# Optimization experiments

Measured on AMD Instinct MI355X. Metric: run time of the kernel, lower is better.

The kernel has to match this reference:

```python
import jax, jax.numpy as jnp
import numpy as np
import math

B, D_MODEL, SEQ_LEN, EMB_DIM, ORDER = 4, 1024, 4096, 5, 64


def setup_inputs() -> dict:
    key = jax.random.key(0)
    ks = jax.random.split(key, 12)
    L = SEQ_LEN
    # PositionalEmbedding: z = [t, Re(e^{-i f w}), Im(e^{-i f w})]
    t = jnp.linspace(0.0, 1.0, L)[None, :, None]                      # [1,L,1]
    bands = (EMB_DIM - 1) // 2
    t_rescaled = jnp.linspace(0.0, L - 1, L)[None, :, None]           # [1,L,1]
    w = 2 * math.pi * t_rescaled / L
    f = jnp.linspace(1e-4, bands - 1, bands)[None, None]              # [1,1,bands]
    zc = jnp.exp(-1j * f * w.astype(jnp.complex64))                   # [1,L,bands]
    z = jnp.concatenate([t, zc.real, zc.imag], axis=-1)               # [1,L,EMB_DIM]
    # ExponentialModulation deltas (fast_decay_pct=0.3, slow_decay_pct=1.5, target=0.01)
    max_decay = math.log(0.01) / 0.3
    min_decay = math.log(0.01) / 1.5
    deltas = jnp.linspace(min_decay, max_decay, D_MODEL)[None, None]  # [1,1,D]
    s = 0.1  # small init scale for MLP weights
    return {
        "x": jax.random.normal(ks[0], (B, D_MODEL, SEQ_LEN), jnp.float32),
        "L": SEQ_LEN,
        "z": z.astype(jnp.float32),
        "t": t.astype(jnp.float32),
        "deltas": deltas.astype(jnp.float32),
        "W1": jax.random.normal(ks[1], (ORDER, EMB_DIM), jnp.float32) * s,
        "b1": jax.random.normal(ks[2], (ORDER,), jnp.float32) * s,
        "freq": jnp.ones((1, ORDER), jnp.float32),  # Sin freq, w=1
        "W2": jax.random.normal(ks[3], (ORDER, ORDER), jnp.float32) * s,
        "b2": jax.random.normal(ks[4], (ORDER,), jnp.float32) * s,
        "W3": jax.random.normal(ks[5], (ORDER, ORDER), jnp.float32) * s,
        "b3": jax.random.normal(ks[6], (ORDER,), jnp.float32) * s,
        "W4": jax.random.normal(ks[7], (D_MODEL, ORDER), jnp.float32) * s,
        "bias": jax.random.normal(ks[8], (D_MODEL,), jnp.float32),
    }


def reference(x, L, z, t, deltas, W1, b1, freq, W2, b2, W3, b3, W4, bias):
    # --- implicit filter MLP: z [1,L,E] -> k [1,L,D] ---
    zL, tL = z[:, :L], t[:, :L]
    h = jnp.sin(freq * (jnp.einsum('ble,oe->blo', zL, W1) + b1))
    h = jnp.sin(freq * (jnp.einsum('blo,po->blp', h, W2) + b2))
    h = jnp.sin(freq * (jnp.einsum('blo,po->blp', h, W3) + b3))
    h = jnp.einsum('blo,do->bld', h, W4)                # [1,L,D], no bias
    # --- exponential modulation ---
    decay = jnp.exp(-tL * jnp.abs(deltas))              # [1,L,D]
    h = h * decay
    k = h[0].T                                          # [D, L] per-channel filters
    # --- FFT causal conv: irfft(rfft(u)*rfft(k)/n, norm='forward') == plain circular conv on 2L ---
    n = 2 * L
    u_f = jnp.fft.rfft(x, n=n)                          # [B,D,L+1] complex
    k_f = jnp.fft.rfft(k, n=n)                          # [D,L+1]
    y = jnp.fft.irfft(u_f * k_f, n=n)[..., :L]          # [B,D,L]
    out = y + x * bias[:, None]                         # D.unsqueeze(-1) bias term, gelu=False
    return out.astype(x.dtype)
```

## Files before the change

kernel.cpp:

```cpp
#include <hip/hip_runtime.h>
#include <math.h>


#define PAD(i) ((i) + ((i) >> 4))
#define TWO_PI 6.2831853071795864769f

typedef float2 cplx;

__device__ __forceinline__ cplx cmul(cplx a, cplx b) {
    return make_float2(a.x * b.x - a.y * b.y, a.x * b.y + a.y * b.x);
}

__device__ __forceinline__ void dft8(cplx v[8], float sgn) {
    cplx t;
    t = v[1]; v[1] = v[4]; v[4] = t;
    t = v[3]; v[3] = v[6]; v[6] = t;
#pragma unroll
    for (int i = 0; i < 8; i += 2) {
        cplx a = v[i], b = v[i + 1];
        v[i]     = make_float2(a.x + b.x, a.y + b.y);
        v[i + 1] = make_float2(a.x - b.x, a.y - b.y);
    }
#pragma unroll
    for (int i = 0; i < 8; i += 4) {
        cplx a = v[i], b = v[i + 2];
        v[i]     = make_float2(a.x + b.x, a.y + b.y);
        v[i + 2] = make_float2(a.x - b.x, a.y - b.y);
        cplx c1 = v[i + 1], d = v[i + 3];
        cplx dt = make_float2(-sgn * d.y, sgn * d.x);
        v[i + 1] = make_float2(c1.x + dt.x, c1.y + dt.y);
        v[i + 3] = make_float2(c1.x - dt.x, c1.y - dt.y);
    }
    const float C = 0.70710678118654752440f;
    cplx a, b, bt;
    a = v[0]; b = v[4];
    v[0] = make_float2(a.x + b.x, a.y + b.y);
    v[4] = make_float2(a.x - b.x, a.y - b.y);
    a = v[1]; b = v[5]; bt = cmul(b, make_float2(C, sgn * C));
    v[1] = make_float2(a.x + bt.x, a.y + bt.y);
    v[5] = make_float2(a.x - bt.x, a.y - bt.y);
    a = v[2]; b = v[6]; bt = make_float2(-sgn * b.y, sgn * b.x);
    v[2] = make_float2(a.x + bt.x, a.y + bt.y);
    v[6] = make_float2(a.x - bt.x, a.y - bt.y);
    a = v[3]; b = v[7]; bt = cmul(b, make_float2(-C, sgn * C));
    v[3] = make_float2(a.x + bt.x, a.y + bt.y);
    v[7] = make_float2(a.x - bt.x, a.y - bt.y);
}

__device__ __forceinline__ void twiddle_powers(float ang, cplx w[8]) {
    float s, c;
    __sincosf(ang, &s, &c);
    w[1] = make_float2(c, s);
    w[2] = cmul(w[1], w[1]);
    w[3] = cmul(w[2], w[1]);
    w[4] = cmul(w[2], w[2]);
    w[5] = cmul(w[4], w[1]);
    w[6] = cmul(w[3], w[3]);
    w[7] = cmul(w[4], w[3]);
}

template <int NS>
__device__ __forceinline__ void fft_pass_ip(cplx* __restrict__ buf, int j, float sgn) {
    cplx* rp = buf + (j + (j >> 4));
    cplx v[8];
#pragma unroll
    for (int r = 0; r < 8; r++) v[r] = rp[544 * r];
    if (NS > 1) {
        int jm = j & (NS - 1);
        float ang = sgn * (TWO_PI / (float)(NS * 8)) * (float)jm;
        cplx w[8];
        twiddle_powers(ang, w);
#pragma unroll
        for (int r = 1; r < 8; r++) v[r] = cmul(v[r], w[r]);
    }
    dft8(v, sgn);
    __syncthreads();
    int base = ((j & ~(NS - 1)) << 3) + (j & (NS - 1));
    cplx* wp = buf + (base + (base >> 4));
#pragma unroll
    for (int r = 0; r < 8; r++) {
        const int off = (NS == 1) ? r
                      : (NS == 8) ? (8 * r + (r >> 1))
                      : (NS == 64) ? (68 * r)
                      : (544 * r);
        wp[off] = v[r];
    }
    __syncthreads();
}

__device__ __forceinline__ void fft_pass1_fwd_regs(cplx* __restrict__ buf, int j,
                                                   const cplx xv[4]) {
    cplx v[8];
#pragma unroll
    for (int r = 0; r < 4; r++) v[r] = xv[r];
#pragma unroll
    for (int r = 4; r < 8; r++) v[r] = make_float2(0.f, 0.f);
    dft8(v, -1.0f);
    int b8 = 8 * j;
    cplx* wp = buf + (b8 + (b8 >> 4));
#pragma unroll
    for (int r = 0; r < 8; r++) wp[r] = v[r];
    __syncthreads();
}

__global__ __launch_bounds__(256) void mlp_kernel(
    const float* __restrict__ zin, const float* __restrict__ W1,
    const float* __restrict__ b1, const float* __restrict__ freq,
    const float* __restrict__ W2, const float* __restrict__ b2,
    const float* __restrict__ W3, const float* __restrict__ b3,
    float* __restrict__ h3T) {
    __shared__ float hs1[64][64];
    __shared__ float hs2[64][64];
    int tid = threadIdx.x;
    int l = tid & 63, w = tid >> 6;
    int lg = blockIdx.x * 64 + l;

    float zf[5];
#pragma unroll
    for (int e = 0; e < 5; e++) zf[e] = zin[lg * 5 + e];

#pragma unroll
    for (int i = 0; i < 16; i++) {
        int o = w * 16 + i;
        float a = b1[o];
#pragma unroll
        for (int e = 0; e < 5; e++) a += W1[o * 5 + e] * zf[e];
        hs1[o][l] = __sinf(freq[o] * a);
    }
    __syncthreads();

    float acc[16];
#pragma unroll
    for (int i = 0; i < 16; i++) acc[i] = b2[w * 16 + i];
#pragma unroll 8
    for (int o = 0; o < 64; o++) {
        float hv = hs1[o][l];
#pragma unroll
        for (int i = 0; i < 16; i++) acc[i] += W2[(w * 16 + i) * 64 + o] * hv;
    }
#pragma unroll
    for (int i = 0; i < 16; i++)
        hs2[w * 16 + i][l] = __sinf(freq[w * 16 + i] * acc[i]);
    __syncthreads();

#pragma unroll
    for (int i = 0; i < 16; i++) acc[i] = b3[w * 16 + i];
#pragma unroll 8
    for (int o = 0; o < 64; o++) {
        float hv = hs2[o][l];
#pragma unroll
        for (int i = 0; i < 16; i++) acc[i] += W3[(w * 16 + i) * 64 + o] * hv;
    }
#pragma unroll
    for (int i = 0; i < 16; i++)
        h3T[(size_t)(w * 16 + i) * 4096 + lg] = __sinf(freq[w * 16 + i] * acc[i]);
}

__global__ __launch_bounds__(256) void kgemm_kernel(
    const float* __restrict__ h3T, const float* __restrict__ W4,
    const float* __restrict__ tvec, const float* __restrict__ deltas,
    float* __restrict__ kout) {
    int lt = blockIdx.x & 3;
    int dt = blockIdx.x >> 2;
    int l0 = lt * 1024 + threadIdx.x * 4;
    float4 acc[16];
#pragma unroll
    for (int i = 0; i < 16; i++) acc[i] = make_float4(0.f, 0.f, 0.f, 0.f);
#pragma unroll 8
    for (int o = 0; o < 64; o++) {
        float4 h = *(const float4*)(h3T + (size_t)o * 4096 + l0);
#pragma unroll
        for (int i = 0; i < 16; i++) {
            float wv = W4[(size_t)(dt * 16 + i) * 64 + o];
            acc[i].x += wv * h.x; acc[i].y += wv * h.y;
            acc[i].z += wv * h.z; acc[i].w += wv * h.w;
        }
    }
    float4 tl = *(const float4*)(tvec + l0);
#pragma unroll
    for (int i = 0; i < 16; i++) {
        int d = dt * 16 + i;
        float da = fabsf(deltas[d]);
        float4 o;
        o.x = acc[i].x * __expf(-tl.x * da);
        o.y = acc[i].y * __expf(-tl.y * da);
        o.z = acc[i].z * __expf(-tl.z * da);
        o.w = acc[i].w * __expf(-tl.w * da);
        *(float4*)(kout + (size_t)d * 4096 + l0) = o;
    }
}

__global__ __launch_bounds__(512) void convf_kernel(
    const float* __restrict__ x, const float* __restrict__ kin,
    const float* __restrict__ bias, float* __restrict__ out) {
    __shared__ cplx buf[4352];
    int d = blockIdx.x;
    int t = threadIdx.x;

    float sb, cb;
    __sincosf(-TWO_PI * (float)t * (1.0f / 8192.0f), &sb, &cb);
    cplx wk[4];
    wk[0] = make_float2(cb, sb);
    wk[1] = cmul(wk[0], make_float2(0.92387953251128675613f, -0.38268343236508977173f));
    wk[2] = cmul(wk[0], make_float2(0.70710678118654752440f, -0.70710678118654752440f));
    wk[3] = cmul(wk[0], make_float2(0.38268343236508977173f, -0.92387953251128675613f));

    cplx* rb  = buf + (t + (t >> 4));
    cplx* qb2 = buf + (((4096 - t) + ((4096 - t) >> 4)) - 1632);

    {
        const cplx* k2 = (const cplx*)(kin + (size_t)d * 4096);
        cplx kv[4];
#pragma unroll
        for (int r = 0; r < 4; r++) kv[r] = k2[t + (r << 9)];
        fft_pass1_fwd_regs(buf, t, kv);
        fft_pass_ip<8>(buf, t, -1.0f);
        fft_pass_ip<64>(buf, t, -1.0f);
        fft_pass_ip<512>(buf, t, -1.0f);
    }
    const float scale = 1.0f / 4096.0f;
    cplx Kk[4], Kq[4], Km = make_float2(0.f, 0.f);
#pragma unroll
    for (int i = 0; i < 4; i++) {
        if (t == 0 && i == 0) {
            cplx z0 = buf[0];
            Kk[0] = make_float2((z0.x + z0.y) * scale, (z0.x - z0.y) * scale);
            cplx zm = buf[PAD(2048)];
            Km = make_float2(zm.x * scale, -zm.y * scale);
            Kq[0] = make_float2(0.f, 0.f);
        } else {
            cplx Zk = rb[544 * i];
            cplx Zq = qb2[544 * (3 - i)];
            cplx Fe = make_float2(0.5f * (Zk.x + Zq.x), 0.5f * (Zk.y - Zq.y));
            cplx Fo = make_float2(0.5f * (Zk.y + Zq.y), -0.5f * (Zk.x - Zq.x));
            cplx WFo = cmul(wk[i], Fo);
            Kk[i] = make_float2((Fe.x + WFo.x) * scale, (Fe.y + WFo.y) * scale);
            Kq[i] = make_float2((Fe.x - WFo.x) * scale, -(Fe.y - WFo.y) * scale);
        }
    }

    float bd = bias[d];
    cplx xv[4], xn[4];
    {
        const cplx* xr = (const cplx*)(x + (size_t)d * 4096);
#pragma unroll
        for (int r = 0; r < 4; r++) xv[r] = xr[t + (r << 9)];
    }

#pragma unroll 1
    for (int b = 0; b < 4; b++) {
        __syncthreads();
        fft_pass1_fwd_regs(buf, t, xv);
        if (b < 3) {
            const cplx* xr = (const cplx*)(x + ((size_t)(b + 1) * 1024 + d) * 4096);
#pragma unroll
            for (int r = 0; r < 4; r++) xn[r] = xr[t + (r << 9)];
        }
        fft_pass_ip<8>(buf, t, -1.0f);
        fft_pass_ip<64>(buf, t, -1.0f);
        fft_pass_ip<512>(buf, t, -1.0f);

#pragma unroll
        for (int i = 0; i < 4; i++) {
            if (t == 0 && i == 0) {
                cplx z0 = buf[0];
                float U0 = z0.x + z0.y;
                float UN = z0.x - z0.y;
                float Y0 = U0 * Kk[0].x;
                float YN = UN * Kk[0].y;
                buf[0] = make_float2(0.5f * (Y0 + YN), 0.5f * (Y0 - YN));
                cplx zm = buf[PAD(2048)];
                cplx Um = make_float2(zm.x, -zm.y);
                cplx Ym = cmul(Um, Km);
                buf[PAD(2048)] = make_float2(Ym.x, -Ym.y);
            } else {
                cplx Zk = rb[544 * i];
                cplx Zq = qb2[544 * (3 - i)];
                cplx Fe = make_float2(0.5f * (Zk.x + Zq.x), 0.5f * (Zk.y - Zq.y));
                cplx Fo = make_float2(0.5f * (Zk.y + Zq.y), -0.5f * (Zk.x - Zq.x));
                cplx WFo = cmul(wk[i], Fo);
                cplx U1 = make_float2(Fe.x + WFo.x, Fe.y + WFo.y);
                cplx U2 = make_float2(Fe.x - WFo.x, -(Fe.y - WFo.y));
                cplx Y1 = cmul(U1, Kk[i]);
                cplx Y2 = cmul(U2, Kq[i]);
                cplx FeY = make_float2(0.5f * (Y1.x + Y2.x), 0.5f * (Y1.y - Y2.y));
                cplx T   = make_float2(0.5f * (Y1.x - Y2.x), 0.5f * (Y1.y + Y2.y));
                cplx FoY = cmul(make_float2(wk[i].x, -wk[i].y), T);
                rb[544 * i]        = make_float2(FeY.x - FoY.y, FeY.y + FoY.x);
                qb2[544 * (3 - i)] = make_float2(FeY.x + FoY.y, FoY.x - FeY.y);
            }
        }
        __syncthreads();

        fft_pass_ip<1>(buf, t, 1.0f);
        fft_pass_ip<8>(buf, t, 1.0f);
        fft_pass_ip<64>(buf, t, 1.0f);
        {
            cplx v[8];
#pragma unroll
            for (int r = 0; r < 8; r++) v[r] = rb[544 * r];
            float ang = (TWO_PI / 4096.0f) * (float)t;
            cplx w[8];
            twiddle_powers(ang, w);
#pragma unroll
            for (int r = 1; r < 8; r++) v[r] = cmul(v[r], w[r]);
            dft8(v, 1.0f);
            cplx* o2 = (cplx*)(out + ((size_t)b * 1024 + d) * 4096);
#pragma unroll
            for (int r = 0; r < 4; r++) {
                cplx o;
                o.x = v[r].x + xv[r].x * bd;
                o.y = v[r].y + xv[r].y * bd;
                o2[t + (r << 9)] = o;
            }
        }
#pragma unroll
        for (int r = 0; r < 4; r++) xv[r] = xn[r];
    }
}

extern "C" void kernel_launch(void* const* d_in, const int* in_sizes, int n_in,
                              void* d_out, int out_size, void* d_ws, size_t ws_size,
                              hipStream_t stream) {
    const float* x      = (const float*)d_in[0];
    const float* zin    = (const float*)d_in[2];
    const float* tvec   = (const float*)d_in[3];
    const float* deltas = (const float*)d_in[4];
    const float* W1     = (const float*)d_in[5];
    const float* b1     = (const float*)d_in[6];
    const float* freq   = (const float*)d_in[7];
    const float* W2     = (const float*)d_in[8];
    const float* b2     = (const float*)d_in[9];
    const float* W3     = (const float*)d_in[10];
    const float* b3     = (const float*)d_in[11];
    const float* W4     = (const float*)d_in[12];
    const float* bias   = (const float*)d_in[13];
    float* out = (float*)d_out;

    float* h3T  = (float*)d_ws;
    float* kbuf = (float*)((char*)d_ws + (size_t)64 * 4096 * sizeof(float));

    mlp_kernel<<<64, 256, 0, stream>>>(zin, W1, b1, freq, W2, b2, W3, b3, h3T);
    kgemm_kernel<<<256, 256, 0, stream>>>(h3T, W4, tvec, deltas, kbuf);
    convf_kernel<<<1024, 512, 0, stream>>>(x, kbuf, bias, out);
}
```

Baseline: 271.8 us.

## Split filter FFT into separate kernel and parallelize convolution over batch rows

The fused per-channel kernel, which transformed the filter and then looped serially over four batch rows, is split in two. A new kernel computes each channel's filter spectrum once and stores it to a global workspace. A second kernel launches one block per (batch, channel) row and reads the spectrum back from global memory. This trades the serial batch loop and register-held spectra for four times more independent blocks, at the cost of extra global memory traffic for writing and re-reading the spectrum, and of an additional launch. The time-domain filter is also staged in the last batch slice of the output buffer.

```diff
diff --git a/kernel.cpp b/kernel.cpp
--- a/kernel.cpp
+++ b/kernel.cpp
@@ -190,13 +190,21 @@
     }
 }
 
-__global__ __launch_bounds__(512) void convf_kernel(
-    const float* __restrict__ x, const float* __restrict__ kin,
-    const float* __restrict__ bias, float* __restrict__ out) {
+__global__ __launch_bounds__(512) void filter_fft_kernel(
+    const float* __restrict__ kin, float2* __restrict__ Kf) {
     __shared__ cplx buf[4352];
-    int d = blockIdx.x;
-    int t = threadIdx.x;
-
+    int d = blockIdx.x, t = threadIdx.x;
+
+    const cplx* k2 = (const cplx*)(kin + (size_t)d * 4096);
+    cplx xv[4];
+#pragma unroll
+    for (int r = 0; r < 4; r++) xv[r] = k2[t + (r << 9)];
+    fft_pass1_fwd_regs(buf, t, xv);
+    fft_pass_ip<8>(buf, t, -1.0f);
+    fft_pass_ip<64>(buf, t, -1.0f);
+    fft_pass_ip<512>(buf, t, -1.0f);
+
+    const float scale = 1.0f / 4096.0f;
     float sb, cb;
     __sincosf(-TWO_PI * (float)t * (1.0f / 8192.0f), &sb, &cb);
     cplx wk[4];
@@ -207,115 +215,114 @@
 
     cplx* rb  = buf + (t + (t >> 4));
     cplx* qb2 = buf + (((4096 - t) + ((4096 - t) >> 4)) - 1632);
-
-    {
-        const cplx* k2 = (const cplx*)(kin + (size_t)d * 4096);
-        cplx kv[4];
-#pragma unroll
-        for (int r = 0; r < 4; r++) kv[r] = k2[t + (r << 9)];
-        fft_pass1_fwd_regs(buf, t, kv);
-        fft_pass_ip<8>(buf, t, -1.0f);
-        fft_pass_ip<64>(buf, t, -1.0f);
-        fft_pass_ip<512>(buf, t, -1.0f);
-    }
-    const float scale = 1.0f / 4096.0f;
-    cplx Kk[4], Kq[4], Km = make_float2(0.f, 0.f);
+    float2* KfRow = Kf + (size_t)d * 4104;
+    float2* kfp = KfRow + t;
+    float2* kfq = KfRow + (4096 - t);
 #pragma unroll
     for (int i = 0; i < 4; i++) {
         if (t == 0 && i == 0) {
             cplx z0 = buf[0];
-            Kk[0] = make_float2((z0.x + z0.y) * scale, (z0.x - z0.y) * scale);
+            KfRow[0]    = make_float2((z0.x + z0.y) * scale, 0.f);
+            KfRow[4096] = make_float2((z0.x - z0.y) * scale, 0.f);
             cplx zm = buf[PAD(2048)];
-            Km = make_float2(zm.x * scale, -zm.y * scale);
-            Kq[0] = make_float2(0.f, 0.f);
+            KfRow[2048] = make_float2(zm.x * scale, -zm.y * scale);
         } else {
             cplx Zk = rb[544 * i];
             cplx Zq = qb2[544 * (3 - i)];
             cplx Fe = make_float2(0.5f * (Zk.x + Zq.x), 0.5f * (Zk.y - Zq.y));
             cplx Fo = make_float2(0.5f * (Zk.y + Zq.y), -0.5f * (Zk.x - Zq.x));
             cplx WFo = cmul(wk[i], Fo);
-            Kk[i] = make_float2((Fe.x + WFo.x) * scale, (Fe.y + WFo.y) * scale);
-            Kq[i] = make_float2((Fe.x - WFo.x) * scale, -(Fe.y - WFo.y) * scale);
+            kfp[512 * i]  = make_float2((Fe.x + WFo.x) * scale, (Fe.y + WFo.y) * scale);
+            kfq[-512 * i] = make_float2((Fe.x - WFo.x) * scale, -(Fe.y - WFo.y) * scale);
         }
     }
-
-    float bd = bias[d];
-    cplx xv[4], xn[4];
+}
+
+__global__ __launch_bounds__(512) void conv_kernel(
+    const float* __restrict__ x, const float2* __restrict__ Kf,
+    const float* __restrict__ bias, float* __restrict__ out) {
+    __shared__ cplx buf[4352];
+    int rid = blockIdx.x;
+    int d = rid & 1023;
+    int t = threadIdx.x;
+
+    const cplx* x2 = (const cplx*)(x + (size_t)rid * 4096);
+    cplx xv[4];
+#pragma unroll
+    for (int r = 0; r < 4; r++) xv[r] = x2[t + (r << 9)];
+    fft_pass1_fwd_regs(buf, t, xv);
+    fft_pass_ip<8>(buf, t, -1.0f);
+    fft_pass_ip<64>(buf, t, -1.0f);
+    fft_pass_ip<512>(buf, t, -1.0f);
+
+    float sb, cb;
+    __sincosf(-TWO_PI * (float)t * (1.0f / 8192.0f), &sb, &cb);
+    cplx wk[4];
+    wk[0] = make_float2(cb, sb);
+    wk[1] = cmul(wk[0], make_float2(0.92387953251128675613f, -0.38268343236508977173f));
+    wk[2] = cmul(wk[0], make_float2(0.70710678118654752440f, -0.70710678118654752440f));
+    wk[3] = cmul(wk[0], make_float2(0.38268343236508977173f, -0.92387953251128675613f));
+
+    cplx* rb  = buf + (t + (t >> 4));
+    cplx* qb2 = buf + (((4096 - t) + ((4096 - t) >> 4)) - 1632);
+    const float2* KfRow = Kf + (size_t)d * 4104;
+    const float2* kfp = KfRow + t;
+    const float2* kfq = KfRow + (4096 - t);
+#pragma unroll
+    for (int i = 0; i < 4; i++) {
+        if (t == 0 && i == 0) {
+            cplx z0 = buf[0];
+            float U0 = z0.x + z0.y;
+            float UN = z0.x - z0.y;
+            float Y0 = U0 * KfRow[0].x;
+            float YN = UN * KfRow[4096].x;
+            buf[0] = make_float2(0.5f * (Y0 + YN), 0.5f * (Y0 - YN));
+            cplx zm = buf[PAD(2048)];
+            cplx Um = make_float2(zm.x, -zm.y);
+            cplx Ym = cmul(Um, KfRow[2048]);
+            buf[PAD(2048)] = make_float2(Ym.x, -Ym.y);
+        } else {
+            cplx Zk = rb[544 * i];
+            cplx Zq = qb2[544 * (3 - i)];
+            cplx K1 = kfp[512 * i], K2 = kfq[-512 * i];
+            cplx Fe = make_float2(0.5f * (Zk.x + Zq.x), 0.5f * (Zk.y - Zq.y));
+            cplx Fo = make_float2(0.5f * (Zk.y + Zq.y), -0.5f * (Zk.x - Zq.x));
+            cplx WFo = cmul(wk[i], Fo);
+            cplx U1 = make_float2(Fe.x + WFo.x, Fe.y + WFo.y);
+            cplx U2 = make_float2(Fe.x - WFo.x, -(Fe.y - WFo.y));
+            cplx Y1 = cmul(U1, K1);
+            cplx Y2 = cmul(U2, K2);
+            cplx FeY = make_float2(0.5f * (Y1.x + Y2.x), 0.5f * (Y1.y - Y2.y));
+            cplx T   = make_float2(0.5f * (Y1.x - Y2.x), 0.5f * (Y1.y + Y2.y));
+            cplx FoY = cmul(make_float2(wk[i].x, -wk[i].y), T);
+            rb[544 * i]        = make_float2(FeY.x - FoY.y, FeY.y + FoY.x);
+            qb2[544 * (3 - i)] = make_float2(FeY.x + FoY.y, FoY.x - FeY.y);
+        }
+    }
+    __syncthreads();
+
+    fft_pass_ip<1>(buf, t, 1.0f);
+    fft_pass_ip<8>(buf, t, 1.0f);
+    fft_pass_ip<64>(buf, t, 1.0f);
     {
-        const cplx* xr = (const cplx*)(x + (size_t)d * 4096);
-#pragma unroll
-        for (int r = 0; r < 4; r++) xv[r] = xr[t + (r << 9)];
-    }
-
-#pragma unroll 1
-    for (int b = 0; b < 4; b++) {
-        __syncthreads();
-        fft_pass1_fwd_regs(buf, t, xv);
-        if (b < 3) {
-            const cplx* xr = (const cplx*)(x + ((size_t)(b + 1) * 1024 + d) * 4096);
-#pragma unroll
-            for (int r = 0; r < 4; r++) xn[r] = xr[t + (r << 9)];
+        cplx v[8];
+#pragma unroll
+        for (int r = 0; r < 8; r++) v[r] = rb[544 * r];
+        float ang = (TWO_PI / 4096.0f) * (float)t;
+        cplx w[8];
+        twiddle_powers(ang, w);
+#pragma unroll
+        for (int r = 1; r < 8; r++) v[r] = cmul(v[r], w[r]);
+        dft8(v, 1.0f);
+        float bd = bias[d];
+        cplx* o2 = (cplx*)(out + (size_t)rid * 4096);
+#pragma unroll
+        for (int r = 0; r < 4; r++) {
+            cplx o;
+            o.x = v[r].x + xv[r].x * bd;
+            o.y = v[r].y + xv[r].y * bd;
+            o2[t + (r << 9)] = o;
         }
-        fft_pass_ip<8>(buf, t, -1.0f);
-        fft_pass_ip<64>(buf, t, -1.0f);
-        fft_pass_ip<512>(buf, t, -1.0f);
-
-#pragma unroll
-        for (int i = 0; i < 4; i++) {
-            if (t == 0 && i == 0) {
-                cplx z0 = buf[0];
-                float U0 = z0.x + z0.y;
-                float UN = z0.x - z0.y;
-                float Y0 = U0 * Kk[0].x;
-                float YN = UN * Kk[0].y;
-                buf[0] = make_float2(0.5f * (Y0 + YN), 0.5f * (Y0 - YN));
-                cplx zm = buf[PAD(2048)];
-                cplx Um = make_float2(zm.x, -zm.y);
-                cplx Ym = cmul(Um, Km);
-                buf[PAD(2048)] = make_float2(Ym.x, -Ym.y);
-            } else {
-                cplx Zk = rb[544 * i];
-                cplx Zq = qb2[544 * (3 - i)];
-                cplx Fe = make_float2(0.5f * (Zk.x + Zq.x), 0.5f * (Zk.y - Zq.y));
-                cplx Fo = make_float2(0.5f * (Zk.y + Zq.y), -0.5f * (Zk.x - Zq.x));
-                cplx WFo = cmul(wk[i], Fo);
-                cplx U1 = make_float2(Fe.x + WFo.x, Fe.y + WFo.y);
-                cplx U2 = make_float2(Fe.x - WFo.x, -(Fe.y - WFo.y));
-                cplx Y1 = cmul(U1, Kk[i]);
-                cplx Y2 = cmul(U2, Kq[i]);
-                cplx FeY = make_float2(0.5f * (Y1.x + Y2.x), 0.5f * (Y1.y - Y2.y));
-                cplx T   = make_float2(0.5f * (Y1.x - Y2.x), 0.5f * (Y1.y + Y2.y));
-                cplx FoY = cmul(make_float2(wk[i].x, -wk[i].y), T);
-                rb[544 * i]        = make_float2(FeY.x - FoY.y, FeY.y + FoY.x);
-                qb2[544 * (3 - i)] = make_float2(FeY.x + FoY.y, FoY.x - FeY.y);
-            }
-        }
-        __syncthreads();
-
-        fft_pass_ip<1>(buf, t, 1.0f);
-        fft_pass_ip<8>(buf, t, 1.0f);
-        fft_pass_ip<64>(buf, t, 1.0f);
-        {
-            cplx v[8];
-#pragma unroll
-            for (int r = 0; r < 8; r++) v[r] = rb[544 * r];
-            float ang = (TWO_PI / 4096.0f) * (float)t;
-            cplx w[8];
-            twiddle_powers(ang, w);
-#pragma unroll
-            for (int r = 1; r < 8; r++) v[r] = cmul(v[r], w[r]);
-            dft8(v, 1.0f);
-            cplx* o2 = (cplx*)(out + ((size_t)b * 1024 + d) * 4096);
-#pragma unroll
-            for (int r = 0; r < 4; r++) {
-                cplx o;
-                o.x = v[r].x + xv[r].x * bd;
-                o.y = v[r].y + xv[r].y * bd;
-                o2[t + (r << 9)] = o;
-            }
-        }
-#pragma unroll
-        for (int r = 0; r < 4; r++) xv[r] = xn[r];
     }
 }
 
@@ -337,10 +344,12 @@
     const float* bias   = (const float*)d_in[13];
     float* out = (float*)d_out;
 
-    float* h3T  = (float*)d_ws;
-    float* kbuf = (float*)((char*)d_ws + (size_t)64 * 4096 * sizeof(float));
+    float*  h3T = (float*)d_ws;
+    float2* Kf  = (float2*)((char*)d_ws + (size_t)64 * 4096 * sizeof(float));
+    float* kbuf = out + (size_t)3072 * 4096;
 
     mlp_kernel<<<64, 256, 0, stream>>>(zin, W1, b1, freq, W2, b2, W3, b3, h3T);
     kgemm_kernel<<<256, 256, 0, stream>>>(h3T, W4, tvec, deltas, kbuf);
-    convf_kernel<<<1024, 512, 0, stream>>>(x, kbuf, bias, out);
-}
+    filter_fft_kernel<<<1024, 512, 0, stream>>>(kbuf, Kf);
+    conv_kernel<<<4096, 512, 0, stream>>>(x, Kf, bias, out);
+}
```

After: 229.8 us. 1.18x faster.
